# Kernel optimization log

Measured on AMD Instinct MI355X. Metric: run time of the kernel, lower is better.

Reference implementation:

```python
import jax, jax.numpy as jnp
import numpy as np

B = 512            # number of graphs in the batch
P = 256            # nodes per graph (== max_graph_size, graphs are equal-sized)
N = B * P          # total nodes
E = 2 * 1024 * 1024
F = 64             # node_feat_size
LAYERS = [32, 32, 32, 1]


def setup_inputs() -> dict:
    key = jax.random.key(0)
    ks = jax.random.split(key, 16)
    x = jax.random.normal(ks[0], (N, F), dtype=jnp.float32)
    edge_index = jax.random.randint(ks[1], (2, E), 0, N, dtype=jnp.int32)
    batch = (jnp.arange(N, dtype=jnp.int32) // P)   # sorted graph ids, equal sizes
    edge_mask = jax.random.uniform(ks[2], (E,), dtype=jnp.float32)
    # layer weights (DGCNN layer: out = D^-1 @ A_tilde @ X @ W + b)
    dims = [F] + LAYERS
    params = {}
    for i in range(len(LAYERS)):
        fan = dims[i]
        params[f"W{i}"] = jax.random.normal(ks[3 + 2 * i], (dims[i], dims[i + 1]), dtype=jnp.float32) / np.sqrt(fan)
        params[f"b{i}"] = jnp.zeros((dims[i + 1],), dtype=jnp.float32)
    return {"x": x, "edge_index": edge_index, "batch": batch, "edge_mask": edge_mask, **params}


def _build_matrices(x, edge_index, batch, edge_mask):
    # counts / exclusive starts per graph (batch is sorted)
    ones = jnp.ones_like(batch)
    counts = jax.ops.segment_sum(ones, batch, num_segments=B)
    starts = jnp.cumsum(counts) - counts                       # [B]
    src, dst = edge_index[0], edge_index[1]
    g = batch[src]
    valid = (batch[src] == batch[dst])                          # drop cross-graph edges
    ls = jnp.clip(src - starts[g], 0, P - 1)
    ld = jnp.clip(dst - starts[g], 0, P - 1)
    w = jnp.where(valid, edge_mask, 0.0)
    # padded A_tilde = A + I  (duplicate edges accumulate, as sparse COO add does)
    adj = jnp.zeros((B, P, P), dtype=x.dtype).at[g, ls, ld].add(w)
    adj = adj + jnp.eye(P, dtype=x.dtype)[None]
    # reciprocal degree of A_tilde, nan/inf -> 0
    deg = adj.sum(axis=2)                                       # [B, P]
    rinv = jnp.where(deg > 0, 1.0 / deg, 0.0)
    feats = x.reshape(B, P, F)                                  # equal-size graphs -> trivial pad
    return adj, rinv, feats


def reference(x, edge_index, batch, edge_mask, W0, b0, W1, b1, W2, b2, W3, b3):
    adj, rinv, h = _build_matrices(x, edge_index, batch, edge_mask)
    for W, b in ((W0, b0), (W1, b1), (W2, b2), (W3, b3)):
        h = jnp.einsum('bnm,bmf->bnf', adj, h @ W)              # A_tilde @ X @ W
        h = rinv[..., None] * h + b                             # D^-1 scaling + bias
        h = jnp.tanh(h)
    return h
```

## Files before the change

### kernel.cpp

```cpp
#include <hip/hip_runtime.h>
#include <hip/hip_bf16.h>

#define BGR 512
#define PP  256
#define NN  (BGR * PP)
#define EE  (2 * 1024 * 1024)
#define RCAP 4

__global__ void k_escatter(const int* __restrict__ ei, const float* __restrict__ emask,
                           int* __restrict__ rowcnt, int2* __restrict__ ebkt) {
    int e0 = (blockIdx.x * 256 + threadIdx.x) * 4;
    int4 s4 = *reinterpret_cast<const int4*>(ei + e0);
    int4 d4 = *reinterpret_cast<const int4*>(ei + EE + e0);
#pragma unroll
    for (int j = 0; j < 4; j++) {
        int s = (&s4.x)[j];
        int d = (&d4.x)[j];
        if ((s >> 8) != (d >> 8)) continue;
        float w = emask[e0 + j];
        int pos = atomicAdd(&rowcnt[s], 1);
        if (pos < RCAP) ebkt[s * RCAP + pos] = make_int2(d & 255, __float_as_int(w));
    }
}

__device__ __forceinline__ float fast_tanh(float x) {
    float t = __expf(2.0f * x);
    return 1.0f - __fdividef(2.0f, 1.0f + t);
}

template <int KH>
__device__ __forceinline__ void pmv32(const float (&h)[KH], const float* __restrict__ W,
                                      float (&P)[32]) {
#pragma unroll
    for (int c = 0; c < 32; c++) P[c] = 0.f;
#pragma unroll
    for (int k = 0; k < KH; k++) {
        const float hk = h[k];
#pragma unroll
        for (int c = 0; c < 32; c++) P[c] += hk * W[k * 32 + c];
    }
}

__global__ __launch_bounds__(512, 4)
void k_fused(const float* __restrict__ x,
             const float* __restrict__ W0, const float* __restrict__ b0,
             const float* __restrict__ W1, const float* __restrict__ b1,
             const float* __restrict__ W2, const float* __restrict__ b2,
             const float* __restrict__ W3, const float* __restrict__ b3,
             const int* __restrict__ rowcnt, const int2* __restrict__ ebkt,
             float* __restrict__ out) {
    __shared__ float Psl[PP][36];

    const int t    = threadIdx.x;
    const int g    = blockIdx.x;
    const int row  = t & 255;
    const int half = __builtin_amdgcn_readfirstlane(t >> 8);
    const int cb   = half * 16;
    const int ob   = 16 - cb;

    const int node = g * PP + row;

    const int cnt = min(rowcnt[node], RCAP);
    int   eld[RCAP];
    float ewt[RCAP];
    float wsum = 0.f;
#pragma unroll
    for (int j = 0; j < RCAP; j++) {
        if (j < cnt) {
            int2 v = ebkt[node * RCAP + j];
            eld[j] = v.x;
            ewt[j] = __int_as_float(v.y);
            wsum += ewt[j];
        } else {
            eld[j] = row;
            ewt[j] = 0.f;
        }
    }
    const float rv = 1.0f / (1.0f + wsum);

    float xr[32];
    const float* xrow = x + (size_t)node * 64 + half * 32;
#pragma unroll
    for (int k = 0; k < 32; k += 4) {
        float4 v = *reinterpret_cast<const float4*>(xrow + k);
        xr[k] = v.x; xr[k + 1] = v.y; xr[k + 2] = v.z; xr[k + 3] = v.w;
    }

    const float* Ws0 = W0 + half * (32 * 32);
    const float* Ws1 = W1 + half * (16 * 32);
    const float* Ws2 = W2 + half * (16 * 32);

    float P[32];
    float acc[16];
    float h[16];

#pragma unroll
    for (int L = 0; L < 3; L++) {
        if (L == 0)      pmv32<32>(xr, Ws0, P);
        else if (L == 1) pmv32<16>(h, Ws1, P);
        else             pmv32<16>(h, Ws2, P);

#pragma unroll
        for (int j = 0; j < 16; j += 4)
            *reinterpret_cast<float4*>(&Psl[row][ob + j]) =
                make_float4(P[ob + j], P[ob + j + 1], P[ob + j + 2], P[ob + j + 3]);
        __syncthreads();

#pragma unroll
        for (int j = 0; j < 16; j += 4) {
            float4 q = *reinterpret_cast<const float4*>(&Psl[row][cb + j]);
            acc[j]     = P[cb + j]     + q.x;
            acc[j + 1] = P[cb + j + 1] + q.y;
            acc[j + 2] = P[cb + j + 2] + q.z;
            acc[j + 3] = P[cb + j + 3] + q.w;
        }
#pragma unroll
        for (int j = 0; j < 16; j += 4)
            *reinterpret_cast<float4*>(&Psl[row][cb + j]) =
                make_float4(acc[j], acc[j + 1], acc[j + 2], acc[j + 3]);
        __syncthreads();

#pragma unroll
        for (int e = 0; e < RCAP; e++) {
            if (ewt[e] != 0.f) {
                int ld = eld[e];
                float w = ewt[e];
#pragma unroll
                for (int j = 0; j < 16; j += 4) {
                    float4 y = *reinterpret_cast<const float4*>(&Psl[ld][cb + j]);
                    acc[j]     += w * y.x;
                    acc[j + 1] += w * y.y;
                    acc[j + 2] += w * y.z;
                    acc[j + 3] += w * y.w;
                }
            }
        }

        const float* b = (L == 0) ? b0 : (L == 1) ? b1 : b2;
#pragma unroll
        for (int j = 0; j < 16; j++) h[j] = fast_tanh(rv * acc[j] + b[cb + j]);
        __syncthreads();
    }

    float a = 0.f;
#pragma unroll
    for (int k = 0; k < 16; k++) a += h[k] * W3[cb + k];
    Psl[row][32 + half] = a;
    __syncthreads();
    if (half == 0) {
        float z = Psl[row][32] + Psl[row][33];
#pragma unroll
        for (int e = 0; e < RCAP; e++) {
            if (ewt[e] != 0.f) {
                int ld = eld[e];
                z += ewt[e] * (Psl[ld][32] + Psl[ld][33]);
            }
        }
        out[node] = fast_tanh(rv * z + b3[0]);
    }
}


extern "C" void kernel_launch(void* const* d_in, const int* in_sizes, int n_in,
                              void* d_out, int out_size, void* d_ws, size_t ws_size,
                              hipStream_t stream) {
    const float* x     = (const float*)d_in[0];
    const int*   ei    = (const int*)d_in[1];
    const float* emask = (const float*)d_in[3];
    const float* W0 = (const float*)d_in[4];
    const float* b0 = (const float*)d_in[5];
    const float* W1 = (const float*)d_in[6];
    const float* b1 = (const float*)d_in[7];
    const float* W2 = (const float*)d_in[8];
    const float* b2 = (const float*)d_in[9];
    const float* W3 = (const float*)d_in[10];
    const float* b3 = (const float*)d_in[11];
    float* out = (float*)d_out;

    int*  rowcnt = (int*)d_ws;
    int2* ebkt   = (int2*)(rowcnt + NN);

    hipMemsetAsync(d_ws, 0, (size_t)NN * sizeof(int), stream);

    k_escatter<<<EE / 1024, 256, 0, stream>>>(ei, emask, rowcnt, ebkt);

    k_fused<<<BGR, 512, 0, stream>>>(x, W0, b0, W1, b1, W2, b2, W3, b3,
                                     rowcnt, ebkt, out);
}
```

Before: 132.1 us.

## Move layer-0 X·W0 projection into the edge-scatter kernel's extra blocks

The edge-scatter kernel gains 512 extra blocks that compute X@W0 per node and write the 32-wide result to workspace, so this dense work runs alongside the atomic-heavy scatter. The fused kernel then starts layer 0 by reading XW rows, including neighbor rows straight from global memory, instead of doing the 64x32 matvec and an LDS exchange. This drops one shared-memory round and two barriers from layer 0 and removes register pressure from the 32-element x row. In exchange it adds a global write and re-read of a 16 MB intermediate, plus scattered neighbor reads from global memory.

```diff
diff --git a/kernel.cpp b/kernel.cpp
--- a/kernel.cpp
+++ b/kernel.cpp
@@ -7,27 +7,66 @@
 #define EE  (2 * 1024 * 1024)
 #define RCAP 4
 
-__global__ void k_escatter(const int* __restrict__ ei, const float* __restrict__ emask,
-                           int* __restrict__ rowcnt, int2* __restrict__ ebkt) {
-    int e0 = (blockIdx.x * 256 + threadIdx.x) * 4;
-    int4 s4 = *reinterpret_cast<const int4*>(ei + e0);
-    int4 d4 = *reinterpret_cast<const int4*>(ei + EE + e0);
-#pragma unroll
-    for (int j = 0; j < 4; j++) {
-        int s = (&s4.x)[j];
-        int d = (&d4.x)[j];
-        if ((s >> 8) != (d >> 8)) continue;
-        float w = emask[e0 + j];
-        int pos = atomicAdd(&rowcnt[s], 1);
-        if (pos < RCAP) ebkt[s * RCAP + pos] = make_int2(d & 255, __float_as_int(w));
-    }
-}
-
 __device__ __forceinline__ float fast_tanh(float x) {
     float t = __expf(2.0f * x);
     return 1.0f - __fdividef(2.0f, 1.0f + t);
 }
 
+__global__ __launch_bounds__(256)
+void k_prep(const int* __restrict__ ei, const float* __restrict__ emask,
+            int* __restrict__ rowcnt, int2* __restrict__ ebkt,
+            const float* __restrict__ x, const float* __restrict__ W0,
+            float* __restrict__ XW) {
+    if (blockIdx.x < 2048) {
+        int e0 = (blockIdx.x * 256 + threadIdx.x) * 4;
+        int4 s4 = *reinterpret_cast<const int4*>(ei + e0);
+        int4 d4 = *reinterpret_cast<const int4*>(ei + EE + e0);
+#pragma unroll
+        for (int j = 0; j < 4; j++) {
+            int s = (&s4.x)[j];
+            int d = (&d4.x)[j];
+            if ((s >> 8) != (d >> 8)) continue;
+            float w = emask[e0 + j];
+            int pos = atomicAdd(&rowcnt[s], 1);
+            if (pos < RCAP) ebkt[s * RCAP + pos] = make_int2(d & 255, __float_as_int(w));
+        }
+    } else {
+        const int node = (blockIdx.x - 2048) * 256 + threadIdx.x;
+        const float* xr = x + (size_t)node * 64;
+        float s0[32], s1[32];
+#pragma unroll
+        for (int c = 0; c < 32; c++) { s0[c] = 0.f; s1[c] = 0.f; }
+#pragma unroll
+        for (int kb = 0; kb < 32; kb += 4) {
+            float4 xq = *reinterpret_cast<const float4*>(xr + kb);
+#pragma unroll
+            for (int j = 0; j < 4; j++) {
+                const float hk = (&xq.x)[j];
+                const int k = kb + j;
+#pragma unroll
+                for (int c = 0; c < 32; c++) s0[c] += hk * W0[k * 32 + c];
+            }
+        }
+#pragma unroll
+        for (int kb = 32; kb < 64; kb += 4) {
+            float4 xq = *reinterpret_cast<const float4*>(xr + kb);
+#pragma unroll
+            for (int j = 0; j < 4; j++) {
+                const float hk = (&xq.x)[j];
+                const int k = kb + j;
+#pragma unroll
+                for (int c = 0; c < 32; c++) s1[c] += hk * W0[k * 32 + c];
+            }
+        }
+        float* o = XW + (size_t)node * 32;
+#pragma unroll
+        for (int c = 0; c < 32; c += 4)
+            *reinterpret_cast<float4*>(o + c) =
+                make_float4(s0[c] + s1[c], s0[c + 1] + s1[c + 1],
+                            s0[c + 2] + s1[c + 2], s0[c + 3] + s1[c + 3]);
+    }
+}
+
 template <int KH>
 __device__ __forceinline__ void pmv32(const float (&h)[KH], const float* __restrict__ W,
                                       float (&P)[32]) {
@@ -42,8 +81,8 @@
 }
 
 __global__ __launch_bounds__(512, 4)
-void k_fused(const float* __restrict__ x,
-             const float* __restrict__ W0, const float* __restrict__ b0,
+void k_fused(const float* __restrict__ XW,
+             const float* __restrict__ b0,
              const float* __restrict__ W1, const float* __restrict__ b1,
              const float* __restrict__ W2, const float* __restrict__ b2,
              const float* __restrict__ W3, const float* __restrict__ b3,
@@ -78,27 +117,44 @@
     }
     const float rv = 1.0f / (1.0f + wsum);
 
-    float xr[32];
-    const float* xrow = x + (size_t)node * 64 + half * 32;
-#pragma unroll
-    for (int k = 0; k < 32; k += 4) {
-        float4 v = *reinterpret_cast<const float4*>(xrow + k);
-        xr[k] = v.x; xr[k + 1] = v.y; xr[k + 2] = v.z; xr[k + 3] = v.w;
-    }
-
-    const float* Ws0 = W0 + half * (32 * 32);
+    float acc[16];
+    float h[16];
+
+    {
+        const float* xwrow = XW + (size_t)node * 32 + cb;
+#pragma unroll
+        for (int j = 0; j < 16; j += 4) {
+            float4 v = *reinterpret_cast<const float4*>(xwrow + j);
+            acc[j] = v.x; acc[j + 1] = v.y; acc[j + 2] = v.z; acc[j + 3] = v.w;
+        }
+#pragma unroll
+        for (int e = 0; e < RCAP; e++) {
+            if (ewt[e] != 0.f) {
+                const float w = ewt[e];
+                const float* nb = XW + (size_t)(g * PP + eld[e]) * 32 + cb;
+#pragma unroll
+                for (int j = 0; j < 16; j += 4) {
+                    float4 y = *reinterpret_cast<const float4*>(nb + j);
+                    acc[j]     += w * y.x;
+                    acc[j + 1] += w * y.y;
+                    acc[j + 2] += w * y.z;
+                    acc[j + 3] += w * y.w;
+                }
+            }
+        }
+#pragma unroll
+        for (int j = 0; j < 16; j++) h[j] = fast_tanh(rv * acc[j] + b0[cb + j]);
+    }
+
     const float* Ws1 = W1 + half * (16 * 32);
     const float* Ws2 = W2 + half * (16 * 32);
 
     float P[32];
-    float acc[16];
-    float h[16];
-
-#pragma unroll
-    for (int L = 0; L < 3; L++) {
-        if (L == 0)      pmv32<32>(xr, Ws0, P);
-        else if (L == 1) pmv32<16>(h, Ws1, P);
-        else             pmv32<16>(h, Ws2, P);
+
+#pragma unroll
+    for (int L = 1; L < 3; L++) {
+        if (L == 1) pmv32<16>(h, Ws1, P);
+        else        pmv32<16>(h, Ws2, P);
 
 #pragma unroll
         for (int j = 0; j < 16; j += 4)
@@ -136,7 +192,7 @@
             }
         }
 
-        const float* b = (L == 0) ? b0 : (L == 1) ? b1 : b2;
+        const float* b = (L == 1) ? b1 : b2;
 #pragma unroll
         for (int j = 0; j < 16; j++) h[j] = fast_tanh(rv * acc[j] + b[cb + j]);
         __syncthreads();
@@ -177,13 +233,14 @@
     const float* b3 = (const float*)d_in[11];
     float* out = (float*)d_out;
 
-    int*  rowcnt = (int*)d_ws;
-    int2* ebkt   = (int2*)(rowcnt + NN);
+    int*   rowcnt = (int*)d_ws;
+    int2*  ebkt   = (int2*)(rowcnt + NN);
+    float* XW     = (float*)(ebkt + (size_t)NN * RCAP);
 
     hipMemsetAsync(d_ws, 0, (size_t)NN * sizeof(int), stream);
 
-    k_escatter<<<EE / 1024, 256, 0, stream>>>(ei, emask, rowcnt, ebkt);
-
-    k_fused<<<BGR, 512, 0, stream>>>(x, W0, b0, W1, b1, W2, b2, W3, b3,
+    k_prep<<<2048 + 512, 256, 0, stream>>>(ei, emask, rowcnt, ebkt, x, W0, XW);
+
+    k_fused<<<BGR, 512, 0, stream>>>(XW, b0, W1, b1, W2, b2, W3, b3,
                                      rowcnt, ebkt, out);
 }
```

New measurement: 144.3 us. +9.2%, slower.
